# Performance work log

Measured on AMD Instinct MI355X. Metric: run time of the kernel, lower is better.

Reference implementation:

```python
import jax, jax.numpy as jnp
import numpy as np

C_WEIGHT = 0.005  # 'c' hyperparameter

def _psi(v):
    return jnp.sign(v) * jnp.log1p(jnp.abs(v))

def setup_inputs() -> dict:
    key = jax.random.key(0)
    ks = jax.random.split(key, 16)
    B, P, C = 64, 128, 72
    s = lambda fan_in: 1.0 / np.sqrt(fan_in)
    return {
        'x': jax.random.normal(ks[0], (B, P, 4), dtype=jnp.float32),
        'h': jax.random.normal(ks[1], (B, P, C), dtype=jnp.float32),
        'We1': jax.random.normal(ks[2], (2 * C + 2, 72), dtype=jnp.float32) * s(2 * C + 2),
        'be1': jnp.zeros((72,), dtype=jnp.float32),
        'We2': jax.random.normal(ks[3], (72, 72), dtype=jnp.float32) * s(72),
        'be2': jnp.zeros((72,), dtype=jnp.float32),
        'Wm': jax.random.normal(ks[4], (72, 1), dtype=jnp.float32) * s(72),
        'bm': jnp.zeros((1,), dtype=jnp.float32),
        'Wh1': jax.random.normal(ks[5], (C + 72, 72), dtype=jnp.float32) * s(C + 72),
        'bh1': jnp.zeros((72,), dtype=jnp.float32),
        'Wh2': jax.random.normal(ks[6], (72, 72), dtype=jnp.float32) * s(72),
        'bh2': jnp.zeros((72,), dtype=jnp.float32),
        'Wx': jax.random.normal(ks[7], (72, 1), dtype=jnp.float32) * s(72),
    }

def reference(x, h, We1, be1, We2, be2, Wm, bm, Wh1, bh1, Wh2, bh2, Wx):
    B, P, _ = x.shape
    # pairwise Minkowski invariants: take(...,0)*2 - sum == t^2 - |vec|^2
    x1 = x[:, :, None, :]  # (B,P,1,4)
    x2 = x[:, None, :, :]  # (B,1,P,4)
    d2 = jnp.square(x1 - x2)                      # (B,P,P,4)
    norms = 2.0 * d2[..., 0] - d2.sum(axis=-1)    # (B,P,P)
    z = x1 * x2
    prods = 2.0 * z[..., 0] - z.sum(axis=-1)      # (B,P,P)
    norms = _psi(norms)[..., None]                # use_psi=True
    prods = _psi(prods)[..., None]
    H = h.shape[-1]
    h1 = jnp.broadcast_to(h[:, :, None, :], (B, P, P, H))
    h2 = jnp.broadcast_to(h[:, None, :, :], (B, P, P, H))
    feat = jnp.concatenate([h1, h2, norms, prods], axis=-1)  # (B,P,P,2H+2)
    # phi_e: two Dense+ReLU
    m = jax.nn.relu(feat @ We1 + be1)
    m = jax.nn.relu(m @ We2 + be2)                # (B,P,P,72)
    # phi_m: Dense(1) + sigmoid
    w = jax.nn.sigmoid(m @ Wm + bm)               # (B,P,P,1)
    wm = jnp.sum(w * m, axis=2)                   # (B,P,72)
    # phi_h: Dense+ReLU, Dense; residual add
    g = jax.nn.relu(jnp.concatenate([h, wm], axis=-1) @ Wh1 + bh1)
    dh = g @ Wh2 + bh2
    h_out = h + dh
    # phi_x: Dense(1, no bias); x update
    phi_x = m @ Wx                                # (B,P,P,1)
    x_out = x + C_WEIGHT * jnp.mean(phi_x * x[:, None, :, :], axis=2)
    return (h_out, x_out)
```

## Files before the change

### kernel.cpp

```cpp
#include <hip/hip_runtime.h>
#include <hip/hip_bf16.h>
#include <math.h>

#define B_ 64
#define P_ 128
#define C_ 72
#define PADC 80
#define IT 4

typedef __attribute__((ext_vector_type(8))) _Float16 half8v;
typedef __attribute__((ext_vector_type(4))) _Float16 half4v;
typedef __attribute__((ext_vector_type(4))) float f32x4;
typedef __attribute__((ext_vector_type(2))) float f32x2;

#define FRAG_WE2  0
#define FRAG_WE1A (15 * 64)
#define FRAG_WE1B (30 * 64)
#define FRAG_WH1  (45 * 64)
#define FRAG_WH2  (70 * 64)
#define NFRAG 85

__device__ __forceinline__ float psi_f(float v) {
    float a = fabsf(v);
    return copysignf(__logf(1.0f + a), v);
}
template <int CTRL>
__device__ __forceinline__ float dpp_add(float v) {
    int s = __builtin_amdgcn_update_dpp(0, __builtin_bit_cast(int, v), CTRL, 0xF, 0xF, true);
    return v + __builtin_bit_cast(float, s);
}
__device__ __forceinline__ float red16(float v) {
    v = dpp_add<0xB1>(v);
    v = dpp_add<0x4E>(v);
    v = dpp_add<0x141>(v);
    v = dpp_add<0x140>(v);
    return v;
}
__device__ __forceinline__ half8v cvt8(const float* p) {
    f32x4 a = *(const f32x4*)p;
    f32x4 b = *(const f32x4*)(p + 4);
    half8v r = {(_Float16)a[0], (_Float16)a[1], (_Float16)a[2], (_Float16)a[3],
                (_Float16)b[0], (_Float16)b[1], (_Float16)b[2], (_Float16)b[3]};
    return r;
}
__device__ __forceinline__ half4v cvt4(const float* p) {
    f32x4 a = *(const f32x4*)p;
    half4v r = {(_Float16)a[0], (_Float16)a[1], (_Float16)a[2], (_Float16)a[3]};
    return r;
}

__global__ __launch_bounds__(64) void setup_kernel(
    const float* __restrict__ We1, const float* __restrict__ be1,
    const float* __restrict__ We2, const float* __restrict__ be2,
    const float* __restrict__ Wh1, const float* __restrict__ bh1,
    const float* __restrict__ Wh2, const float* __restrict__ bh2,
    half8v* __restrict__ frags)
{
    const int bid = blockIdx.x;
    const int l = threadIdx.x;
    const int c16 = l & 15, g = l >> 4;

    if (bid >= NFRAG) {
        half4v* tail = (half4v*)(frags + NFRAG * 64);
        const int nt = bid - NFRAG;
        const int n = nt * 16 + c16;
        half4v f = {};
        if (n < C_) {
            #pragma unroll
            for (int jj = 0; jj < 4; ++jj) {
                int k = 64 + 4 * g + jj;
                float w = 0.f;
                if (k < C_) w = We2[k * C_ + n];
                else if (k == C_) w = be2[n];
                f[jj] = (_Float16)w;
            }
        }
        tail[nt * 64 + l] = f;
        return;
    }

    const float* W;
    const float* bias;
    int kmax, rel;
    if (bid < 15)      { W = We2;            bias = be2;     kmax = 72;  rel = bid; }
    else if (bid < 30) { W = We1;            bias = nullptr; kmax = 72;  rel = bid - 15; }
    else if (bid < 45) { W = We1 + 72 * C_;  bias = be1;     kmax = 72;  rel = bid - 30; }
    else if (bid < 70) { W = Wh1;            bias = bh1;     kmax = 144; rel = bid - 45; }
    else               { W = Wh2;            bias = bh2;     kmax = 72;  rel = bid - 70; }
    const int kt = rel / 5, nt = rel - 5 * kt;
    const int n = nt * 16 + c16;

    half8v f = {};
    if (n < C_) {
        #pragma unroll
        for (int jj = 0; jj < 8; ++jj) {
            int k = kt * 32 + g * 8 + jj;
            float w = 0.f;
            if (k < kmax) w = W[k * C_ + n];
            else if (k == kmax && bias) w = bias[n];
            f[jj] = (_Float16)w;
        }
    }
    frags[bid * 64 + l] = f;
}

__global__ __launch_bounds__(64) void pre_kernel(
    const float* __restrict__ h, const half8v* __restrict__ frags,
    _Float16* __restrict__ Ah, half8v* __restrict__ Bcf,
    half4v* __restrict__ Bcft)
{
    __shared__ _Float16 T[16][88];
    const int l = threadIdx.x, c16 = l & 15, g = l >> 4;
    const int sel = blockIdx.x & 1;
    const int m0 = (blockIdx.x >> 1) * 16;

    const float* hrow = h + (m0 + c16) * C_;
    half8v a0 = cvt8(hrow + g * 8);
    half8v a1 = cvt8(hrow + 32 + g * 8);
    half8v a2 = {};
    if (g == 0) a2 = cvt8(hrow + 64);
    else if (g == 1) a2[0] = (_Float16)1.0f;

    const half8v* F = frags + (sel ? FRAG_WE1B : FRAG_WE1A);
    f32x4 acc[5] = {};
    #pragma unroll
    for (int kt = 0; kt < 3; ++kt) {
        half8v a = (kt == 0) ? a0 : (kt == 1 ? a1 : a2);
        #pragma unroll
        for (int nt = 0; nt < 5; ++nt)
            acc[nt] = __builtin_amdgcn_mfma_f32_16x16x32_f16(a, F[(kt * 5 + nt) * 64 + l], acc[nt], 0, 0, 0);
    }

    if (sel == 0) {
        #pragma unroll
        for (int nt = 0; nt < 5; ++nt) {
            int n = nt * 16 + c16;
            if (n < C_) {
                #pragma unroll
                for (int r = 0; r < 4; ++r)
                    Ah[(m0 + 4 * g + r) * PADC + n] = (_Float16)acc[nt][r];
            }
        }
    } else {
        #pragma unroll
        for (int nt = 0; nt < 5; ++nt) {
            int n = nt * 16 + c16;
            if (n < C_) {
                #pragma unroll
                for (int r = 0; r < 4; ++r)
                    T[4 * g + r][n] = (_Float16)acc[nt][r];
            }
        }
        {
            int zr = l >> 2, zc = 72 + (l & 3) * 4;
            half4v z = {};
            *(half4v*)&T[zr][zc] = z;
        }
        __syncthreads();
        const int bb = m0 >> 7, jt = (m0 >> 4) & 7;
        half8v f0 = *(const half8v*)&T[c16][g * 8];
        half8v f1 = *(const half8v*)&T[c16][32 + g * 8];
        half4v ft = *(const half4v*)&T[c16][64 + g * 4];
        Bcf[((bb * 8 + jt) * 2 + 0) * 64 + l] = f0;
        Bcf[((bb * 8 + jt) * 2 + 1) * 64 + l] = f1;
        Bcft[(bb * 8 + jt) * 64 + l] = ft;
    }
}

__global__ __launch_bounds__(256, 2) void edge_kernel(
    const float* __restrict__ x, const _Float16* __restrict__ Ah,
    const half8v* __restrict__ Bcf, const half4v* __restrict__ Bcft,
    const float* __restrict__ We1, const half8v* __restrict__ frags,
    const float* __restrict__ Wm, const float* __restrict__ bm,
    const float* __restrict__ Wx,
    float* __restrict__ wm_out, float* __restrict__ xacc_out)
{
    const int b  = blockIdx.x >> 5;
    const int it = blockIdx.x & 31;
    const int t  = threadIdx.x;
    const int wv = t >> 6;
    const int l  = t & 63;
    const int c16 = l & 15;
    const int g   = l >> 4;

    half8v Wf[2][5];
    #pragma unroll
    for (int kt = 0; kt < 2; ++kt)
        #pragma unroll
        for (int nt = 0; nt < 5; ++nt)
            Wf[kt][nt] = frags[FRAG_WE2 + (kt * 5 + nt) * 64 + l];
    half4v Wf2[5];
    {
        const half4v* tail = (const half4v*)(frags + NFRAG * 64);
        #pragma unroll
        for (int nt = 0; nt < 5; ++nt)
            Wf2[nt] = tail[nt * 64 + l];
    }

    f32x2 WmWx[5][4];
    #pragma unroll
    for (int nt = 0; nt < 5; ++nt)
        #pragma unroll
        for (int r = 0; r < 4; ++r) {
            int ch = nt * 16 + 4 * g + r;
            bool ok = ch < C_;
            WmWx[nt][r][0] = ok ? Wm[ch] : 0.f;
            WmWx[nt][r][1] = ok ? Wx[ch] : 0.f;
        }
    const float bm0 = bm[0];
    const f32x4 zero4 = {0.f, 0.f, 0.f, 0.f};

    const float* w1g = We1 + 144 * C_;
    const float* w2g = We1 + 145 * C_;
    half8v w1a = cvt8(w1g + g * 8);
    half8v w1b = cvt8(w1g + 32 + g * 8);
    half8v w2a = cvt8(w2g + g * 8);
    half8v w2b = cvt8(w2g + 32 + g * 8);
    half4v w1t = {}, w2t = {};
    if (g < 2) { w1t = cvt4(w1g + 64 + g * 4); w2t = cvt4(w2g + 64 + g * 4); }

    const int i = it * IT + wv;
    const int node_i = b * P_ + i;
    const f32x4 xi = *(const f32x4*)&x[node_i * 4];
    const _Float16* Arow = Ah + node_i * PADC;
    half8v a0 = *(const half8v*)&Arow[g * 8];
    half8v a1 = *(const half8v*)&Arow[32 + g * 8];
    half4v at = {};
    if (g < 2) at = *(const half4v*)&Arow[64 + g * 4];

    const half8v* Bb = Bcf + (size_t)(b * 8) * 2 * 64;
    const half4v* Bt = Bcft + (size_t)(b * 8) * 64;
    const float*  xb = x + b * P_ * 4;

    half8v bc0 = Bb[l];
    half8v bc1 = Bb[64 + l];
    half4v bct = Bt[l];
    f32x4 xjv = *(const f32x4*)&xb[c16 * 4];

    f32x4 wmacc[5] = {};
    f32x4 xacc = {0.f, 0.f, 0.f, 0.f};

    #pragma unroll 1
    for (int jt = 0; jt < 8; ++jt) {
        const int njt = (jt + 1) & 7;
        half8v nbc0 = Bb[(njt * 2) * 64 + l];
        half8v nbc1 = Bb[(njt * 2 + 1) * 64 + l];
        half4v nbct = Bt[njt * 64 + l];
        f32x4 nxjv = *(const f32x4*)&xb[(njt * 16 + c16) * 4];

        float d0 = xi[0] - xjv[0], d1 = xi[1] - xjv[1];
        float d2 = xi[2] - xjv[2], d3 = xi[3] - xjv[3];
        float nn = d0 * d0 - d1 * d1 - d2 * d2 - d3 * d3;
        float pp = xi[0] * xjv[0] - xi[1] * xjv[1] - xi[2] * xjv[2] - xi[3] * xjv[3];
        _Float16 nh = (_Float16)psi_f(nn);
        _Float16 ph = (_Float16)psi_f(pp);
        half8v n8 = {nh, nh, nh, nh, nh, nh, nh, nh};
        half8v p8 = {ph, ph, ph, ph, ph, ph, ph, ph};
        half8v zero8 = {};

        half8v af0, af1;
        {
            half8v v = a0 + bc0;
            v = __builtin_elementwise_fma(w1a, n8, v);
            v = __builtin_elementwise_fma(w2a, p8, v);
            af0 = __builtin_elementwise_max(v, zero8);
            half8v u = a1 + bc1;
            u = __builtin_elementwise_fma(w1b, n8, u);
            u = __builtin_elementwise_fma(w2b, p8, u);
            af1 = __builtin_elementwise_max(u, zero8);
        }
        half4v af2 = {};
        if (g < 2) {
            half4v n4 = {nh, nh, nh, nh};
            half4v p4 = {ph, ph, ph, ph};
            half4v zero4h = {};
            half4v v = at + bct;
            v = __builtin_elementwise_fma(w1t, n4, v);
            v = __builtin_elementwise_fma(w2t, p4, v);
            af2 = __builtin_elementwise_max(v, zero4h);
        } else if (g == 2) {
            af2[0] = (_Float16)1.0f;
        }

        f32x4 acc[5] = {};
        #pragma unroll
        for (int nt = 0; nt < 5; ++nt)
            acc[nt] = __builtin_amdgcn_mfma_f32_16x16x32_f16(Wf[0][nt], af0, acc[nt], 0, 0, 0);
        #pragma unroll
        for (int nt = 0; nt < 5; ++nt)
            acc[nt] = __builtin_amdgcn_mfma_f32_16x16x32_f16(Wf[1][nt], af1, acc[nt], 0, 0, 0);
        #pragma unroll
        for (int nt = 0; nt < 5; ++nt)
            acc[nt] = __builtin_amdgcn_mfma_f32_16x16x16f16(Wf2[nt], af2, acc[nt], 0, 0, 0);

        f32x2 wdpd = {0.f, 0.f};
        #pragma unroll
        for (int nt = 0; nt < 5; ++nt) {
            f32x4 m2q = __builtin_elementwise_max(acc[nt], zero4);
            acc[nt] = m2q;
            #pragma unroll
            for (int r = 0; r < 4; ++r) {
                f32x2 vv = {m2q[r], m2q[r]};
                wdpd = __builtin_elementwise_fma(vv, WmWx[nt][r], wdpd);
            }
        }
        {
            f32x2 s;
            s[0] = __shfl_xor(wdpd[0], 16, 64);
            s[1] = __shfl_xor(wdpd[1], 16, 64);
            wdpd += s;
            s[0] = __shfl_xor(wdpd[0], 32, 64);
            s[1] = __shfl_xor(wdpd[1], 32, 64);
            wdpd += s;
        }
        float w_ = __builtin_amdgcn_rcpf(1.f + __expf(-(wdpd[0] + bm0)));
        f32x4 w4 = {w_, w_, w_, w_};
        #pragma unroll
        for (int nt = 0; nt < 5; ++nt)
            wmacc[nt] = __builtin_elementwise_fma(w4, acc[nt], wmacc[nt]);
        f32x4 pd4 = {wdpd[1], wdpd[1], wdpd[1], wdpd[1]};
        xacc = __builtin_elementwise_fma(pd4, xjv, xacc);

        bc0 = nbc0; bc1 = nbc1; bct = nbct; xjv = nxjv;
    }

    #pragma unroll
    for (int nt = 0; nt < 5; ++nt)
        #pragma unroll
        for (int r = 0; r < 4; ++r)
            wmacc[nt][r] = red16(wmacc[nt][r]);
    #pragma unroll
    for (int q = 0; q < 4; ++q) xacc[q] = red16(xacc[q]);

    if (c16 == 0) {
        #pragma unroll
        for (int nt = 0; nt < 5; ++nt)
            #pragma unroll
            for (int r = 0; r < 4; ++r) {
                int ch = nt * 16 + 4 * g + r;
                if (ch < C_) wm_out[node_i * C_ + ch] = wmacc[nt][r];
            }
    }
    if (l == 0)
        *(f32x4*)&xacc_out[node_i * 4] = xacc;
}

__global__ __launch_bounds__(64) void node_kernel(
    const float* __restrict__ x, const float* __restrict__ h,
    const half8v* __restrict__ frags,
    const float* __restrict__ wm, const float* __restrict__ xacc,
    float* __restrict__ hout, float* __restrict__ xout)
{
    __shared__ _Float16 g_s[16][88];
    const int l = threadIdx.x, c16 = l & 15, g = l >> 4;
    const int m0 = blockIdx.x * 16;

    const float* hrow  = h  + (m0 + c16) * C_;
    const float* wmrow = wm + (m0 + c16) * C_;

    half8v a[5];
    #pragma unroll
    for (int kt = 0; kt < 5; ++kt) {
        int k = kt * 32 + g * 8;
        half8v v = {};
        if (k < C_) v = cvt8(hrow + k);
        else if (k < 144) v = cvt8(wmrow + (k - C_));
        else if (k == 144) v[0] = (_Float16)1.0f;
        a[kt] = v;
    }
    f32x4 acc1[5] = {};
    #pragma unroll
    for (int kt = 0; kt < 5; ++kt)
        #pragma unroll
        for (int nt = 0; nt < 5; ++nt)
            acc1[nt] = __builtin_amdgcn_mfma_f32_16x16x32_f16(
                a[kt], frags[FRAG_WH1 + (kt * 5 + nt) * 64 + l], acc1[nt], 0, 0, 0);

    #pragma unroll
    for (int nt = 0; nt < 5; ++nt) {
        int n = nt * 16 + c16;
        #pragma unroll
        for (int r = 0; r < 4; ++r)
            g_s[4 * g + r][n] = (_Float16)fmaxf(acc1[nt][r], 0.f);
    }
    __syncthreads();
    half8v b0 = *(const half8v*)&g_s[c16][g * 8];
    half8v b1 = *(const half8v*)&g_s[c16][32 + g * 8];
    half8v b2 = {};
    if (g == 0) b2 = *(const half8v*)&g_s[c16][64];
    else if (g == 1) b2[0] = (_Float16)1.0f;

    f32x4 acc2[5] = {};
    #pragma unroll
    for (int kt = 0; kt < 3; ++kt) {
        half8v aa = (kt == 0) ? b0 : (kt == 1 ? b1 : b2);
        #pragma unroll
        for (int nt = 0; nt < 5; ++nt)
            acc2[nt] = __builtin_amdgcn_mfma_f32_16x16x32_f16(
                aa, frags[FRAG_WH2 + (kt * 5 + nt) * 64 + l], acc2[nt], 0, 0, 0);
    }
    #pragma unroll
    for (int nt = 0; nt < 5; ++nt) {
        int n = nt * 16 + c16;
        if (n < C_) {
            #pragma unroll
            for (int r = 0; r < 4; ++r) {
                int row = m0 + 4 * g + r;
                hout[row * C_ + n] = h[row * C_ + n] + acc2[nt][r];
            }
        }
    }
    {
        int row = m0 + (l >> 2), d = l & 3;
        xout[row * 4 + d] = x[row * 4 + d] + 0.005f * (xacc[row * 4 + d] * (1.0f / 128.f));
    }
}

extern "C" void kernel_launch(void* const* d_in, const int* in_sizes, int n_in,
                              void* d_out, int out_size, void* d_ws, size_t ws_size,
                              hipStream_t stream) {
    const float* x   = (const float*)d_in[0];
    const float* h   = (const float*)d_in[1];
    const float* We1 = (const float*)d_in[2];
    const float* be1 = (const float*)d_in[3];
    const float* We2 = (const float*)d_in[4];
    const float* be2 = (const float*)d_in[5];
    const float* Wm  = (const float*)d_in[6];
    const float* bm  = (const float*)d_in[7];
    const float* Wh1 = (const float*)d_in[8];
    const float* bh1 = (const float*)d_in[9];
    const float* Wh2 = (const float*)d_in[10];
    const float* bh2 = (const float*)d_in[11];
    const float* Wx  = (const float*)d_in[12];

    const int NNODE = B_ * P_;
    _Float16* Ah  = (_Float16*)d_ws;
    half8v* Bcf   = (half8v*)(Ah + NNODE * PADC);
    half4v* Bcft  = (half4v*)(Bcf + B_ * 8 * 2 * 64);
    float* wm     = (float*)(Bcft + B_ * 8 * 64);
    float* xacc   = wm + NNODE * C_;
    half8v* frags = (half8v*)(xacc + NNODE * 4);

    float* hout = (float*)d_out;
    float* xout = hout + NNODE * C_;

    setup_kernel<<<NFRAG + 5, 64, 0, stream>>>(We1, be1, We2, be2, Wh1, bh1, Wh2, bh2, frags);
    pre_kernel<<<NNODE / 16 * 2, 64, 0, stream>>>(h, frags, Ah, Bcf, Bcft);
    edge_kernel<<<B_ * 32, 256, 0, stream>>>(x, Ah, Bcf, Bcft, We1, frags,
                                             Wm, bm, Wx, wm, xacc);
    node_kernel<<<NNODE / 16, 64, 0, stream>>>(x, h, frags, wm, xacc, hout, xout);
}
```

Baseline: 60.30 us.

## Compute pair geometry once per lane and distribute it with ds_bpermute

The edge kernel now computes the psi(norm) and psi(prod) invariants for 64 distinct j per lane at once, in two passes, instead of 16 values replicated across lane groups every j-tile. The two halves are packed as fp16 and distributed to each tile with ds_bpermute, which cuts redundant log evaluations. Other changes: the We1 geometry rows are pre-converted to fp16 in setup, the bias-one column is folded into Ah padding to drop branches, and the Wm/Wx dot product is split into two accumulators. The cost is extra permute instructions and a small loop restructure.

```diff
diff --git a/kernel.cpp b/kernel.cpp
--- a/kernel.cpp
+++ b/kernel.cpp
@@ -41,11 +41,6 @@
     f32x4 b = *(const f32x4*)(p + 4);
     half8v r = {(_Float16)a[0], (_Float16)a[1], (_Float16)a[2], (_Float16)a[3],
                 (_Float16)b[0], (_Float16)b[1], (_Float16)b[2], (_Float16)b[3]};
-    return r;
-}
-__device__ __forceinline__ half4v cvt4(const float* p) {
-    f32x4 a = *(const f32x4*)p;
-    half4v r = {(_Float16)a[0], (_Float16)a[1], (_Float16)a[2], (_Float16)a[3]};
     return r;
 }
 
@@ -60,6 +55,14 @@
     const int l = threadIdx.x;
     const int c16 = l & 15, g = l >> 4;
 
+    if (bid == NFRAG + 5) {
+        _Float16* w12p = (_Float16*)((half4v*)(frags + NFRAG * 64) + 5 * 64);
+        for (int i = l; i < 160; i += 64) {
+            int s = i / 80, c = i - s * 80;
+            w12p[i] = (c < C_) ? (_Float16)We1[(144 + s) * C_ + c] : (_Float16)0.f;
+        }
+        return;
+    }
     if (bid >= NFRAG) {
         half4v* tail = (half4v*)(frags + NFRAG * 64);
         const int nt = bid - NFRAG;
@@ -141,6 +144,12 @@
                     Ah[(m0 + 4 * g + r) * PADC + n] = (_Float16)acc[nt][r];
             }
         }
+        if (l < 16) {
+            half4v one = {(_Float16)1.0f, (_Float16)0.f, (_Float16)0.f, (_Float16)0.f};
+            half4v z = {};
+            *(half4v*)&Ah[(m0 + l) * PADC + 72] = one;
+            *(half4v*)&Ah[(m0 + l) * PADC + 76] = z;
+        }
     } else {
         #pragma unroll
         for (int nt = 0; nt < 5; ++nt) {
@@ -170,7 +179,7 @@
 __global__ __launch_bounds__(256, 2) void edge_kernel(
     const float* __restrict__ x, const _Float16* __restrict__ Ah,
     const half8v* __restrict__ Bcf, const half4v* __restrict__ Bcft,
-    const float* __restrict__ We1, const half8v* __restrict__ frags,
+    const half8v* __restrict__ frags,
     const float* __restrict__ Wm, const float* __restrict__ bm,
     const float* __restrict__ Wx,
     float* __restrict__ wm_out, float* __restrict__ xacc_out)
@@ -190,12 +199,18 @@
         for (int nt = 0; nt < 5; ++nt)
             Wf[kt][nt] = frags[FRAG_WE2 + (kt * 5 + nt) * 64 + l];
     half4v Wf2[5];
-    {
-        const half4v* tail = (const half4v*)(frags + NFRAG * 64);
-        #pragma unroll
-        for (int nt = 0; nt < 5; ++nt)
-            Wf2[nt] = tail[nt * 64 + l];
-    }
+    const half4v* tail = (const half4v*)(frags + NFRAG * 64);
+    #pragma unroll
+    for (int nt = 0; nt < 5; ++nt)
+        Wf2[nt] = tail[nt * 64 + l];
+
+    const _Float16* w12p = (const _Float16*)(tail + 5 * 64);
+    half8v w1a = *(const half8v*)&w12p[g * 8];
+    half8v w1b = *(const half8v*)&w12p[32 + g * 8];
+    half4v w1t = *(const half4v*)&w12p[64 + g * 4];
+    half8v w2a = *(const half8v*)&w12p[80 + g * 8];
+    half8v w2b = *(const half8v*)&w12p[80 + 32 + g * 8];
+    half4v w2t = *(const half4v*)&w12p[80 + 64 + g * 4];
 
     f32x2 WmWx[5][4];
     #pragma unroll
@@ -209,15 +224,6 @@
         }
     const float bm0 = bm[0];
     const f32x4 zero4 = {0.f, 0.f, 0.f, 0.f};
-
-    const float* w1g = We1 + 144 * C_;
-    const float* w2g = We1 + 145 * C_;
-    half8v w1a = cvt8(w1g + g * 8);
-    half8v w1b = cvt8(w1g + 32 + g * 8);
-    half8v w2a = cvt8(w2g + g * 8);
-    half8v w2b = cvt8(w2g + 32 + g * 8);
-    half4v w1t = {}, w2t = {};
-    if (g < 2) { w1t = cvt4(w1g + 64 + g * 4); w2t = cvt4(w2g + 64 + g * 4); }
 
     const int i = it * IT + wv;
     const int node_i = b * P_ + i;
@@ -225,8 +231,7 @@
     const _Float16* Arow = Ah + node_i * PADC;
     half8v a0 = *(const half8v*)&Arow[g * 8];
     half8v a1 = *(const half8v*)&Arow[32 + g * 8];
-    half4v at = {};
-    if (g < 2) at = *(const half4v*)&Arow[64 + g * 4];
+    half4v at = *(const half4v*)&Arow[64 + g * 4];
 
     const half8v* Bb = Bcf + (size_t)(b * 8) * 2 * 64;
     const half4v* Bt = Bcft + (size_t)(b * 8) * 64;
@@ -235,93 +240,103 @@
     half8v bc0 = Bb[l];
     half8v bc1 = Bb[64 + l];
     half4v bct = Bt[l];
-    f32x4 xjv = *(const f32x4*)&xb[c16 * 4];
 
     f32x4 wmacc[5] = {};
     f32x4 xacc = {0.f, 0.f, 0.f, 0.f};
+    const int c16_4 = c16 << 2;
 
     #pragma unroll 1
-    for (int jt = 0; jt < 8; ++jt) {
-        const int njt = (jt + 1) & 7;
-        half8v nbc0 = Bb[(njt * 2) * 64 + l];
-        half8v nbc1 = Bb[(njt * 2 + 1) * 64 + l];
-        half4v nbct = Bt[njt * 64 + l];
-        f32x4 nxjv = *(const f32x4*)&xb[(njt * 16 + c16) * 4];
-
-        float d0 = xi[0] - xjv[0], d1 = xi[1] - xjv[1];
-        float d2 = xi[2] - xjv[2], d3 = xi[3] - xjv[3];
+    for (int q = 0; q < 2; ++q) {
+        f32x4 xjq = *(const f32x4*)&xb[(q * 64 + l) * 4];
+        float d0 = xi[0] - xjq[0], d1 = xi[1] - xjq[1];
+        float d2 = xi[2] - xjq[2], d3 = xi[3] - xjq[3];
         float nn = d0 * d0 - d1 * d1 - d2 * d2 - d3 * d3;
-        float pp = xi[0] * xjv[0] - xi[1] * xjv[1] - xi[2] * xjv[2] - xi[3] * xjv[3];
-        _Float16 nh = (_Float16)psi_f(nn);
-        _Float16 ph = (_Float16)psi_f(pp);
-        half8v n8 = {nh, nh, nh, nh, nh, nh, nh, nh};
-        half8v p8 = {ph, ph, ph, ph, ph, ph, ph, ph};
-        half8v zero8 = {};
-
-        half8v af0, af1;
-        {
-            half8v v = a0 + bc0;
-            v = __builtin_elementwise_fma(w1a, n8, v);
-            v = __builtin_elementwise_fma(w2a, p8, v);
-            af0 = __builtin_elementwise_max(v, zero8);
-            half8v u = a1 + bc1;
-            u = __builtin_elementwise_fma(w1b, n8, u);
-            u = __builtin_elementwise_fma(w2b, p8, u);
-            af1 = __builtin_elementwise_max(u, zero8);
-        }
-        half4v af2 = {};
-        if (g < 2) {
+        float pp = xi[0] * xjq[0] - xi[1] * xjq[1] - xi[2] * xjq[2] - xi[3] * xjq[3];
+        unsigned geo =
+            (unsigned)__builtin_bit_cast(unsigned short, (_Float16)psi_f(nn)) |
+            ((unsigned)__builtin_bit_cast(unsigned short, (_Float16)psi_f(pp)) << 16);
+        int geo0 = __builtin_amdgcn_ds_bpermute(c16_4,       (int)geo);
+        int geo1 = __builtin_amdgcn_ds_bpermute(c16_4 + 64,  (int)geo);
+        int geo2 = __builtin_amdgcn_ds_bpermute(c16_4 + 128, (int)geo);
+        int geo3 = __builtin_amdgcn_ds_bpermute(c16_4 + 192, (int)geo);
+
+        #pragma unroll
+        for (int s = 0; s < 4; ++s) {
+            const int jt = q * 4 + s;
+            const int njt = (jt + 1) & 7;
+            half8v nbc0 = Bb[(njt * 2) * 64 + l];
+            half8v nbc1 = Bb[(njt * 2 + 1) * 64 + l];
+            half4v nbct = Bt[njt * 64 + l];
+            f32x4 xjv = *(const f32x4*)&xb[(jt * 16 + c16) * 4];
+
+            int geos = (s == 0) ? geo0 : (s == 1) ? geo1 : (s == 2) ? geo2 : geo3;
+            _Float16 nh = __builtin_bit_cast(_Float16, (unsigned short)((unsigned)geos & 0xFFFFu));
+            _Float16 ph = __builtin_bit_cast(_Float16, (unsigned short)((unsigned)geos >> 16));
+            half8v n8 = {nh, nh, nh, nh, nh, nh, nh, nh};
+            half8v p8 = {ph, ph, ph, ph, ph, ph, ph, ph};
             half4v n4 = {nh, nh, nh, nh};
             half4v p4 = {ph, ph, ph, ph};
+            half8v zero8 = {};
             half4v zero4h = {};
-            half4v v = at + bct;
-            v = __builtin_elementwise_fma(w1t, n4, v);
-            v = __builtin_elementwise_fma(w2t, p4, v);
-            af2 = __builtin_elementwise_max(v, zero4h);
-        } else if (g == 2) {
-            af2[0] = (_Float16)1.0f;
-        }
-
-        f32x4 acc[5] = {};
-        #pragma unroll
-        for (int nt = 0; nt < 5; ++nt)
-            acc[nt] = __builtin_amdgcn_mfma_f32_16x16x32_f16(Wf[0][nt], af0, acc[nt], 0, 0, 0);
-        #pragma unroll
-        for (int nt = 0; nt < 5; ++nt)
-            acc[nt] = __builtin_amdgcn_mfma_f32_16x16x32_f16(Wf[1][nt], af1, acc[nt], 0, 0, 0);
-        #pragma unroll
-        for (int nt = 0; nt < 5; ++nt)
-            acc[nt] = __builtin_amdgcn_mfma_f32_16x16x16f16(Wf2[nt], af2, acc[nt], 0, 0, 0);
-
-        f32x2 wdpd = {0.f, 0.f};
-        #pragma unroll
-        for (int nt = 0; nt < 5; ++nt) {
-            f32x4 m2q = __builtin_elementwise_max(acc[nt], zero4);
-            acc[nt] = m2q;
-            #pragma unroll
-            for (int r = 0; r < 4; ++r) {
-                f32x2 vv = {m2q[r], m2q[r]};
-                wdpd = __builtin_elementwise_fma(vv, WmWx[nt][r], wdpd);
-            }
-        }
-        {
-            f32x2 s;
-            s[0] = __shfl_xor(wdpd[0], 16, 64);
-            s[1] = __shfl_xor(wdpd[1], 16, 64);
-            wdpd += s;
-            s[0] = __shfl_xor(wdpd[0], 32, 64);
-            s[1] = __shfl_xor(wdpd[1], 32, 64);
-            wdpd += s;
-        }
-        float w_ = __builtin_amdgcn_rcpf(1.f + __expf(-(wdpd[0] + bm0)));
-        f32x4 w4 = {w_, w_, w_, w_};
-        #pragma unroll
-        for (int nt = 0; nt < 5; ++nt)
-            wmacc[nt] = __builtin_elementwise_fma(w4, acc[nt], wmacc[nt]);
-        f32x4 pd4 = {wdpd[1], wdpd[1], wdpd[1], wdpd[1]};
-        xacc = __builtin_elementwise_fma(pd4, xjv, xacc);
-
-        bc0 = nbc0; bc1 = nbc1; bct = nbct; xjv = nxjv;
+
+            half8v v0 = a0 + bc0;
+            v0 = __builtin_elementwise_fma(w1a, n8, v0);
+            v0 = __builtin_elementwise_fma(w2a, p8, v0);
+            half8v af0 = __builtin_elementwise_max(v0, zero8);
+            half8v v1 = a1 + bc1;
+            v1 = __builtin_elementwise_fma(w1b, n8, v1);
+            v1 = __builtin_elementwise_fma(w2b, p8, v1);
+            half8v af1 = __builtin_elementwise_max(v1, zero8);
+            half4v vt = at + bct;
+            vt = __builtin_elementwise_fma(w1t, n4, vt);
+            vt = __builtin_elementwise_fma(w2t, p4, vt);
+            half4v af2 = __builtin_elementwise_max(vt, zero4h);
+
+            f32x4 acc[5] = {};
+            #pragma unroll
+            for (int nt = 0; nt < 5; ++nt)
+                acc[nt] = __builtin_amdgcn_mfma_f32_16x16x32_f16(Wf[0][nt], af0, acc[nt], 0, 0, 0);
+            #pragma unroll
+            for (int nt = 0; nt < 5; ++nt)
+                acc[nt] = __builtin_amdgcn_mfma_f32_16x16x32_f16(Wf[1][nt], af1, acc[nt], 0, 0, 0);
+            #pragma unroll
+            for (int nt = 0; nt < 5; ++nt)
+                acc[nt] = __builtin_amdgcn_mfma_f32_16x16x16f16(Wf2[nt], af2, acc[nt], 0, 0, 0);
+
+            f32x2 wdA = {0.f, 0.f}, wdB = {0.f, 0.f};
+            #pragma unroll
+            for (int nt = 0; nt < 5; ++nt) {
+                f32x4 m2q = __builtin_elementwise_max(acc[nt], zero4);
+                acc[nt] = m2q;
+                f32x2 e0 = {m2q[0], m2q[0]};
+                f32x2 e1 = {m2q[1], m2q[1]};
+                f32x2 e2 = {m2q[2], m2q[2]};
+                f32x2 e3 = {m2q[3], m2q[3]};
+                wdA = __builtin_elementwise_fma(e0, WmWx[nt][0], wdA);
+                wdB = __builtin_elementwise_fma(e1, WmWx[nt][1], wdB);
+                wdA = __builtin_elementwise_fma(e2, WmWx[nt][2], wdA);
+                wdB = __builtin_elementwise_fma(e3, WmWx[nt][3], wdB);
+            }
+            f32x2 wdpd = wdA + wdB;
+            {
+                f32x2 sx;
+                sx[0] = __shfl_xor(wdpd[0], 16, 64);
+                sx[1] = __shfl_xor(wdpd[1], 16, 64);
+                wdpd += sx;
+                sx[0] = __shfl_xor(wdpd[0], 32, 64);
+                sx[1] = __shfl_xor(wdpd[1], 32, 64);
+                wdpd += sx;
+            }
+            float w_ = __builtin_amdgcn_rcpf(1.f + __expf(-(wdpd[0] + bm0)));
+            f32x4 w4 = {w_, w_, w_, w_};
+            #pragma unroll
+            for (int nt = 0; nt < 5; ++nt)
+                wmacc[nt] = __builtin_elementwise_fma(w4, acc[nt], wmacc[nt]);
+            f32x4 pd4 = {wdpd[1], wdpd[1], wdpd[1], wdpd[1]};
+            xacc = __builtin_elementwise_fma(pd4, xjv, xacc);
+
+            bc0 = nbc0; bc1 = nbc1; bct = nbct;
+        }
     }
 
     #pragma unroll
@@ -444,9 +459,9 @@
     float* hout = (float*)d_out;
     float* xout = hout + NNODE * C_;
 
-    setup_kernel<<<NFRAG + 5, 64, 0, stream>>>(We1, be1, We2, be2, Wh1, bh1, Wh2, bh2, frags);
+    setup_kernel<<<NFRAG + 6, 64, 0, stream>>>(We1, be1, We2, be2, Wh1, bh1, Wh2, bh2, frags);
     pre_kernel<<<NNODE / 16 * 2, 64, 0, stream>>>(h, frags, Ah, Bcf, Bcft);
-    edge_kernel<<<B_ * 32, 256, 0, stream>>>(x, Ah, Bcf, Bcft, We1, frags,
+    edge_kernel<<<B_ * 32, 256, 0, stream>>>(x, Ah, Bcf, Bcft, frags,
                                              Wm, bm, Wx, wm, xacc);
     node_kernel<<<NNODE / 16, 64, 0, stream>>>(x, h, frags, wm, xacc, hout, xout);
 }
```

Measured after the change: 57.24 us. -5.1%, faster.
